# Kernel optimization log

Hardware: AMD Instinct MI355X
Metric: run time of the kernel (lower is better)

The kernel has to match this reference:

```python
import jax, jax.numpy as jnp
import numpy as np

N_NODES = 100000
N_EDGES = 1600000
IN_C, HID_C, OUT_C = 128, 256, 128


def setup_inputs() -> dict:
    key = jax.random.key(0)
    ks = jax.random.split(key, 6)
    x = jax.random.normal(ks[0], (N_NODES, IN_C), dtype=jnp.float32)
    edge_index = jax.random.randint(ks[1], (2, N_EDGES), 0, N_NODES, dtype=jnp.int64)
    s = 0.05
    W1a = jax.random.normal(ks[2], (IN_C, HID_C), dtype=jnp.float32) * s
    b1a = jnp.zeros((HID_C,), dtype=jnp.float32)
    W2a = jax.random.normal(ks[3], (HID_C, HID_C), dtype=jnp.float32) * s
    b2a = jnp.zeros((HID_C,), dtype=jnp.float32)
    W1b = jax.random.normal(ks[4], (HID_C, HID_C), dtype=jnp.float32) * s
    b1b = jnp.zeros((HID_C,), dtype=jnp.float32)
    W2b = jax.random.normal(ks[5], (HID_C, OUT_C), dtype=jnp.float32) * s
    b2b = jnp.zeros((OUT_C,), dtype=jnp.float32)
    return {"x": x, "edge_index": edge_index, "W1a": W1a, "b1a": b1a,
            "W2a": W2a, "b2a": b2a, "W1b": W1b, "b1b": b1b,
            "W2b": W2b, "b2b": b2b}


def _gin_conv(x, src, dst, W1, b1, W2, b2):
    # GINConv (eps=0): nn( x + sum_{j in N(i)} x_j )
    agg = jax.ops.segment_sum(x[src], dst, num_segments=N_NODES)  # [N, d]
    h = x + agg
    h = jnp.maximum(h @ W1 + b1, 0.0)
    return h @ W2 + b2


def reference(x, edge_index, W1a, b1a, W2a, b2a, W1b, b1b, W2b, b2b):
    src, dst = edge_index[0], edge_index[1]
    h = jnp.maximum(_gin_conv(x, src, dst, W1a, b1a, W2a, b2a), 0.0)  # relu(conv1)
    # dropout is identity in eval mode
    out = _gin_conv(h, src, dst, W1b, b1b, W2b, b2b)  # conv2
    return out
```

## Files before the change

kernel.cpp:

```cpp
#include <hip/hip_runtime.h>


#define N_NODES 100000
#define N_EDGES 1600000
#define NBUCK 13

typedef unsigned short ushort_t;
typedef short bf16x8 __attribute__((ext_vector_type(8)));
typedef float floatx4 __attribute__((ext_vector_type(4)));

static __device__ __forceinline__ ushort_t f2bf(float f) {
    unsigned u = __float_as_uint(f);
    u = (u + 0x7FFFu + ((u >> 16) & 1u)) >> 16;
    return (ushort_t)u;
}
static __device__ __forceinline__ unsigned pack2bf(float lo, float hi) {
    return (unsigned)f2bf(lo) | ((unsigned)f2bf(hi) << 16);
}
static __device__ __forceinline__ void addu4(float* acc, const uint4 v) {
    const unsigned w0 = v.x, w1 = v.y, w2 = v.z, w3 = v.w;
    acc[0] += __uint_as_float(w0 << 16);
    acc[1] += __uint_as_float(w0 & 0xFFFF0000u);
    acc[2] += __uint_as_float(w1 << 16);
    acc[3] += __uint_as_float(w1 & 0xFFFF0000u);
    acc[4] += __uint_as_float(w2 << 16);
    acc[5] += __uint_as_float(w2 & 0xFFFF0000u);
    acc[6] += __uint_as_float(w3 << 16);
    acc[7] += __uint_as_float(w3 & 0xFFFF0000u);
}

#define GLOAD_LDS16(g, l)                                                     \
    __builtin_amdgcn_global_load_lds(                                         \
        (const __attribute__((address_space(1))) void*)(g),                   \
        (__attribute__((address_space(3))) void*)(l), 16, 0, 0)

#define NX8 (N_NODES * 128 / 8)
__global__ __launch_bounds__(256) void cvt_fused_kernel(
    const float* __restrict__ X, ushort_t* __restrict__ Xb,
    const float* __restrict__ W1a, const float* __restrict__ W2a,
    const float* __restrict__ W1b, const float* __restrict__ W2b,
    ushort_t* __restrict__ wt1a, ushort_t* __restrict__ wt2a,
    ushort_t* __restrict__ wt1b, ushort_t* __restrict__ wt2b) {
    int i = blockIdx.x * 256 + threadIdx.x;
    if (i < NX8) {
        const float4 a = ((const float4*)X)[2 * i];
        const float4 b = ((const float4*)X)[2 * i + 1];
        uint4 r;
        r.x = pack2bf(a.x, a.y);
        r.y = pack2bf(a.z, a.w);
        r.z = pack2bf(b.x, b.y);
        r.w = pack2bf(b.z, b.w);
        ((uint4*)Xb)[i] = r;
        return;
    }
    i -= NX8;
    if (i < 32768) {
        int k = i >> 8, n = i & 255;
        wt1a[n * 128 + k] = f2bf(W1a[i]);
    } else if (i < 98304) {
        int j = i - 32768, k = j >> 8, n = j & 255;
        wt2a[n * 256 + k] = f2bf(W2a[j]);
    } else if (i < 163840) {
        int j = i - 98304, k = j >> 8, n = j & 255;
        wt1b[n * 256 + k] = f2bf(W1b[j]);
    } else if (i < 196608) {
        int j = i - 163840, k = j >> 7, n = j & 127;
        wt2b[n * 256 + k] = f2bf(W2b[j]);
    }
}

__global__ __launch_bounds__(256) void hist_kernel(const int* __restrict__ src,
                                                   const int* __restrict__ dst,
                                                   int* __restrict__ deg, int nE) {
    for (int e = blockIdx.x * 256 + threadIdx.x; e < nE; e += gridDim.x * 256) {
        int d = dst[e];
        int s = src[e];
        if ((unsigned)d < (unsigned)N_NODES && (unsigned)s < (unsigned)N_NODES)
            atomicAdd(&deg[d], 1);
    }
}

__global__ __launch_bounds__(256) void fill_kernel(const int* __restrict__ src,
                                                   const int* __restrict__ dst,
                                                   int* __restrict__ cursor,
                                                   int* __restrict__ csr_src, int nE) {
    const int bucket = blockIdx.y;
    for (int e = blockIdx.x * 256 + threadIdx.x; e < nE; e += gridDim.x * 256) {
        int d = dst[e];
        int s = src[e];
        if ((unsigned)d < (unsigned)N_NODES && (unsigned)s < (unsigned)N_NODES &&
            (d >> 13) == bucket) {
            int pos = atomicAdd(&cursor[d], 1);
            csr_src[pos] = s;
        }
    }
}

__global__ __launch_bounds__(256) void scan1_kernel(const int* __restrict__ deg,
                                                    int* __restrict__ bsum, int n) {
    __shared__ int l[256];
    int b = blockIdx.x, t = threadIdx.x;
    int base = b * 1024 + t * 4;
    int s = 0;
#pragma unroll
    for (int k = 0; k < 4; ++k) {
        int i = base + k;
        if (i < n) s += deg[i];
    }
    l[t] = s;
    __syncthreads();
    for (int off = 128; off > 0; off >>= 1) {
        if (t < off) l[t] += l[t + off];
        __syncthreads();
    }
    if (t == 0) bsum[b] = l[0];
}

__global__ __launch_bounds__(128) void scan2_kernel(const int* __restrict__ bsum,
                                                    int* __restrict__ boff, int nb) {
    __shared__ int l[128];
    int t = threadIdx.x;
    int v = (t < nb) ? bsum[t] : 0;
    l[t] = v;
    __syncthreads();
    for (int off = 1; off < 128; off <<= 1) {
        int add = (t >= off) ? l[t - off] : 0;
        __syncthreads();
        l[t] += add;
        __syncthreads();
    }
    if (t < nb) boff[t] = l[t] - v;
}

__global__ __launch_bounds__(256) void scan3_kernel(const int* __restrict__ deg,
                                                    const int* __restrict__ boff,
                                                    int* __restrict__ row_ptr,
                                                    int* __restrict__ cursor, int n) {
    __shared__ int l[256];
    int b = blockIdx.x, t = threadIdx.x;
    int base = b * 1024 + t * 4;
    int d[4];
    int s = 0;
#pragma unroll
    for (int k = 0; k < 4; ++k) {
        int i = base + k;
        d[k] = (i < n) ? deg[i] : 0;
        s += d[k];
    }
    l[t] = s;
    __syncthreads();
    for (int off = 1; off < 256; off <<= 1) {
        int add = (t >= off) ? l[t - off] : 0;
        __syncthreads();
        l[t] += add;
        __syncthreads();
    }
    int run = boff[b] + l[t] - s;
#pragma unroll
    for (int k = 0; k < 4; ++k) {
        int i = base + k;
        if (i < n) {
            row_ptr[i] = run;
            cursor[i] = run;
        }
        run += d[k];
    }
}

template <int C, int U>
__global__ __launch_bounds__(256) void agg_gather_kernel(
    const ushort_t* __restrict__ X, ushort_t* __restrict__ T,
    const int* __restrict__ row_ptr, const int* __restrict__ deg,
    const int* __restrict__ csr_src, const ushort_t* __restrict__ zrow, int nN) {
    constexpr int G = C / 8;
    constexpr int NPW = 64 / G;
    constexpr int B = U * NPW;
    const int lane = threadIdx.x & 63;
    const int wid = threadIdx.x >> 6;
    const int node = blockIdx.x * 4 + wid;
    if (node >= nN) return;
    const int sub = lane / G;
    const int coff = (lane % G) * 8;

    float acc[8];
#pragma unroll
    for (int k = 0; k < 8; ++k) acc[k] = 0.f;

    const int base = row_ptr[node];
    const int dg = deg[node];
    for (int j0 = 0; j0 < dg; j0 += 64) {
        int cnt = dg - j0;
        if (cnt > 64) cnt = 64;
        int nidx = (lane < cnt) ? csr_src[base + j0 + lane] : 0;
        if ((unsigned)nidx >= (unsigned)N_NODES) nidx = 0;
        for (int j = 0; j < cnt; j += B) {
            uint4 v[U];
#pragma unroll
            for (int u = 0; u < U; ++u) {
                int jj = j + u * NPW + sub;
                bool ok = jj < cnt;
                int idx = __shfl(nidx, ok ? jj : 0);
                const ushort_t* p = ok ? (X + (size_t)idx * C) : zrow;
                v[u] = *(const uint4*)(p + coff);
            }
#pragma unroll
            for (int u = 0; u < U; ++u) addu4(acc, v[u]);
        }
    }
    if (sub == 0) {
        uint4 v = *(const uint4*)(X + (size_t)node * C + coff);
        addu4(acc, v);
    }
#pragma unroll
    for (int off = G; off < 64; off <<= 1)
#pragma unroll
        for (int k = 0; k < 8; ++k) acc[k] += __shfl_xor(acc[k], off);

    if (lane < G) {
        uint4 r;
        r.x = pack2bf(acc[0], acc[1]);
        r.y = pack2bf(acc[2], acc[3]);
        r.z = pack2bf(acc[4], acc[5]);
        r.w = pack2bf(acc[6], acc[7]);
        *(uint4*)(T + (size_t)node * C + coff) = r;
    }
}

template <int K1, int N2, bool RELU2, typename OT>
__global__ __launch_bounds__(256, 3) void mlp_kernel(
    const ushort_t* __restrict__ A, const ushort_t* __restrict__ Wt1,
    const float* __restrict__ b1, const ushort_t* __restrict__ Wt2,
    const float* __restrict__ b2, OT* __restrict__ C, int M) {
    constexpr int N1 = 256, BM = 64, BK = 32;
    constexpr int NPW2 = N2 / 4;
    constexpr int RN2 = NPW2 / 16;
    __shared__ ushort_t As[BM * BK];
    __shared__ ushort_t Bs[N1 * BK];
    __shared__ ushort_t U[BM * N1];

    const int lane = threadIdx.x & 63;
    const int wid = threadIdx.x >> 6;
    const int l15 = lane & 15;
    const int q = lane >> 4;
    const int srow = lane >> 2;
    const int scol = (lane & 3) * 8;
    const int bm = blockIdx.x * BM;

    floatx4 acc[4][4];
#pragma unroll
    for (int mi = 0; mi < 4; ++mi)
#pragma unroll
        for (int ni = 0; ni < 4; ++ni) {
            floatx4 z = {0.f, 0.f, 0.f, 0.f};
            acc[mi][ni] = z;
        }

    for (int kt = 0; kt < K1; kt += BK) {
        {
            const int gr = bm + wid * 16 + srow;
            if (gr < M)
                GLOAD_LDS16(A + (size_t)gr * K1 + kt + scol, &As[(wid * 16) * BK]);
        }
#pragma unroll
        for (int u = 0; u < 4; ++u) {
            const int row = wid * 64 + u * 16;
            GLOAD_LDS16(Wt1 + (size_t)(row + srow) * K1 + kt + scol, &Bs[row * BK]);
        }
        __syncthreads();
        bf16x8 av[4], bv[4];
#pragma unroll
        for (int mi = 0; mi < 4; ++mi)
            av[mi] = *(const bf16x8*)&Bs[(wid * 64 + mi * 16 + l15) * BK + q * 8];
#pragma unroll
        for (int ni = 0; ni < 4; ++ni)
            bv[ni] = *(const bf16x8*)&As[(ni * 16 + l15) * BK + q * 8];
#pragma unroll
        for (int mi = 0; mi < 4; ++mi)
#pragma unroll
            for (int ni = 0; ni < 4; ++ni)
                acc[mi][ni] = __builtin_amdgcn_mfma_f32_16x16x32_bf16(
                    av[mi], bv[ni], acc[mi][ni], 0, 0, 0);
        __syncthreads();
    }

#pragma unroll
    for (int mi = 0; mi < 4; ++mi) {
        const int h0 = wid * 64 + mi * 16 + q * 4;
        const float4 b4 = *(const float4*)&b1[h0];
#pragma unroll
        for (int ni = 0; ni < 4; ++ni) {
            const int node = ni * 16 + l15;
            float v0 = acc[mi][ni][0] + b4.x; v0 = v0 > 0.f ? v0 : 0.f;
            float v1 = acc[mi][ni][1] + b4.y; v1 = v1 > 0.f ? v1 : 0.f;
            float v2 = acc[mi][ni][2] + b4.z; v2 = v2 > 0.f ? v2 : 0.f;
            float v3 = acc[mi][ni][3] + b4.w; v3 = v3 > 0.f ? v3 : 0.f;
            uint2 w;
            w.x = pack2bf(v0, v1);
            w.y = pack2bf(v2, v3);
            int byte = node * (N1 * 2) + h0 * 2;
            byte ^= (node & 7) << 4;
            *(uint2*)((char*)U + byte) = w;
        }
    }
    __syncthreads();

#pragma unroll
    for (int mi = 0; mi < 4; ++mi)
#pragma unroll
        for (int ni = 0; ni < 4; ++ni) {
            floatx4 z = {0.f, 0.f, 0.f, 0.f};
            acc[mi][ni] = z;
        }

    for (int kt = 0; kt < N1; kt += BK) {
#pragma unroll
        for (int u = 0; u < RN2; ++u) {
            const int row = wid * NPW2 + u * 16;
            GLOAD_LDS16(Wt2 + (size_t)(row + srow) * N1 + kt + scol, &Bs[row * BK]);
        }
        __syncthreads();
        bf16x8 av[4], bv[RN2];
#pragma unroll
        for (int mi = 0; mi < 4; ++mi) {
            const int node = mi * 16 + l15;
            const int byte =
                (node * (N1 * 2) + kt * 2 + q * 16) ^ ((node & 7) << 4);
            av[mi] = *(const bf16x8*)((const char*)U + byte);
        }
#pragma unroll
        for (int ni = 0; ni < RN2; ++ni)
            bv[ni] = *(const bf16x8*)&Bs[(wid * NPW2 + ni * 16 + l15) * BK + q * 8];
#pragma unroll
        for (int mi = 0; mi < 4; ++mi)
#pragma unroll
            for (int ni = 0; ni < RN2; ++ni)
                acc[mi][ni] = __builtin_amdgcn_mfma_f32_16x16x32_bf16(
                    av[mi], bv[ni], acc[mi][ni], 0, 0, 0);
        __syncthreads();
    }

    float bval[RN2];
#pragma unroll
    for (int ni = 0; ni < RN2; ++ni) bval[ni] = b2[wid * NPW2 + ni * 16 + l15];
#pragma unroll
    for (int mi = 0; mi < 4; ++mi) {
#pragma unroll
        for (int r = 0; r < 4; ++r) {
            const int row = bm + mi * 16 + q * 4 + r;
            if (row < M) {
#pragma unroll
                for (int ni = 0; ni < RN2; ++ni) {
                    const int col = wid * NPW2 + ni * 16 + l15;
                    float v = acc[mi][ni][r] + bval[ni];
                    if (RELU2) v = v > 0.f ? v : 0.f;
                    if constexpr (sizeof(OT) == 2)
                        C[(size_t)row * N2 + col] = f2bf(v);
                    else
                        C[(size_t)row * N2 + col] = v;
                }
            }
        }
    }
}

extern "C" void kernel_launch(void* const* d_in, const int* in_sizes, int n_in,
                              void* d_out, int out_size, void* d_ws, size_t ws_size,
                              hipStream_t stream) {
    const float* x   = (const float*)d_in[0];
    const int*   ei  = (const int*)d_in[1];
    const float* W1a = (const float*)d_in[2];
    const float* b1a = (const float*)d_in[3];
    const float* W2a = (const float*)d_in[4];
    const float* b2a = (const float*)d_in[5];
    const float* W1b = (const float*)d_in[6];
    const float* b1b = (const float*)d_in[7];
    const float* W2b = (const float*)d_in[8];
    const float* b2b = (const float*)d_in[9];
    const int* src = ei;
    const int* dst = ei + N_EDGES;
    float* out = (float*)d_out;

    char* base = (char*)d_ws;
    size_t o = 0;
    ushort_t* wt1a = (ushort_t*)(base + o); o += 128 * 256 * 2;
    ushort_t* wt2a = (ushort_t*)(base + o); o += 256 * 256 * 2;
    ushort_t* wt1b = (ushort_t*)(base + o); o += 256 * 256 * 2;
    ushort_t* wt2b = (ushort_t*)(base + o); o += 256 * 128 * 2;
    o = (o + 255) & ~(size_t)255;
    ushort_t* zrow = (ushort_t*)(base + o); o += 512;
    int* deg     = (int*)(base + o); o += (size_t)N_NODES * 4;
    int* row_ptr = (int*)(base + o); o += (size_t)N_NODES * 4;
    int* cursor  = (int*)(base + o); o += (size_t)N_NODES * 4;
    int* bsum    = (int*)(base + o); o += 128 * 4;
    int* boff    = (int*)(base + o); o += 128 * 4;
    o = (o + 255) & ~(size_t)255;
    int* csr_src = (int*)(base + o); o += (size_t)N_EDGES * 4;
    o = (o + 255) & ~(size_t)255;
    ushort_t* t1   = (ushort_t*)(base + o); o += (size_t)N_NODES * 128 * 2;
    ushort_t* tbig = (ushort_t*)(base + o); o += (size_t)N_NODES * 256 * 2;
    o += 128 * 1024;
    (void)ws_size; (void)o; (void)in_sizes; (void)n_in; (void)out_size;

    ushort_t* inter = (ushort_t*)d_out;
    ushort_t* xb    = (ushort_t*)d_out;

    cvt_fused_kernel<<<(NX8 + 196608 + 255) / 256, 256, 0, stream>>>(
        x, xb, W1a, W2a, W1b, W2b, wt1a, wt2a, wt1b, wt2b);

    const int NB = (N_NODES + 1023) / 1024;
    hipMemsetAsync(zrow, 0, 512 + (size_t)N_NODES * 4, stream);
    hist_kernel<<<2048, 256, 0, stream>>>(src, dst, deg, N_EDGES);
    scan1_kernel<<<NB, 256, 0, stream>>>(deg, bsum, N_NODES);
    scan2_kernel<<<1, 128, 0, stream>>>(bsum, boff, NB);
    scan3_kernel<<<NB, 256, 0, stream>>>(deg, boff, row_ptr, cursor, N_NODES);
    fill_kernel<<<dim3(1024, NBUCK), 256, 0, stream>>>(src, dst, cursor, csr_src,
                                                       N_EDGES);

    const int ga = (N_NODES + 3) / 4;
    const int gf = (N_NODES + 63) / 64;

    agg_gather_kernel<128, 4><<<ga, 256, 0, stream>>>(xb, t1, row_ptr, deg,
                                                      csr_src, zrow, N_NODES);
    mlp_kernel<128, 256, true, ushort_t><<<gf, 256, 0, stream>>>(
        t1, wt1a, b1a, wt2a, b2a, inter, N_NODES);

    agg_gather_kernel<256, 8><<<ga, 256, 0, stream>>>(inter, tbig, row_ptr,
                                                      deg, csr_src, zrow, N_NODES);
    mlp_kernel<256, 128, false, float><<<gf, 256, 0, stream>>>(
        tbig, wt1b, b1b, wt2b, b2b, out, N_NODES);
}
```

Measured before the change: 532.4 us.

## Fuse histogram into convert kernel, merge scan passes, pack row_ptr/deg, raise gather unroll

Folds the degree histogram into the fused convert kernel and merges scan2 into scan3, with each block reducing the preceding block sums itself. This removes two kernel launches. It also stores row_ptr and degree as a packed int2 so the gather kernels do one load per node, and doubles the gather unroll factor (U) for both layers to keep more loads in flight. The trade-off is that every scan3 block redundantly re-reduces the block sums, and the higher unroll raises register pressure.

```diff
diff --git a/kernel.cpp b/kernel.cpp
--- a/kernel.cpp
+++ b/kernel.cpp
@@ -35,12 +35,16 @@
         (__attribute__((address_space(3))) void*)(l), 16, 0, 0)
 
 #define NX8 (N_NODES * 128 / 8)
+#define CVT_TOTAL (NX8 + 196608)
+#define HIST_THREADS (2048 * 256)
 __global__ __launch_bounds__(256) void cvt_fused_kernel(
     const float* __restrict__ X, ushort_t* __restrict__ Xb,
     const float* __restrict__ W1a, const float* __restrict__ W2a,
     const float* __restrict__ W1b, const float* __restrict__ W2b,
     ushort_t* __restrict__ wt1a, ushort_t* __restrict__ wt2a,
-    ushort_t* __restrict__ wt1b, ushort_t* __restrict__ wt2b) {
+    ushort_t* __restrict__ wt1b, ushort_t* __restrict__ wt2b,
+    const int* __restrict__ src, const int* __restrict__ dst,
+    int* __restrict__ deg, int nE) {
     int i = blockIdx.x * 256 + threadIdx.x;
     if (i < NX8) {
         const float4 a = ((const float4*)X)[2 * i];
@@ -53,26 +57,24 @@
         ((uint4*)Xb)[i] = r;
         return;
     }
-    i -= NX8;
-    if (i < 32768) {
-        int k = i >> 8, n = i & 255;
-        wt1a[n * 128 + k] = f2bf(W1a[i]);
-    } else if (i < 98304) {
-        int j = i - 32768, k = j >> 8, n = j & 255;
-        wt2a[n * 256 + k] = f2bf(W2a[j]);
-    } else if (i < 163840) {
-        int j = i - 98304, k = j >> 8, n = j & 255;
-        wt1b[n * 256 + k] = f2bf(W1b[j]);
-    } else if (i < 196608) {
-        int j = i - 163840, k = j >> 7, n = j & 127;
-        wt2b[n * 256 + k] = f2bf(W2b[j]);
-    }
-}
-
-__global__ __launch_bounds__(256) void hist_kernel(const int* __restrict__ src,
-                                                   const int* __restrict__ dst,
-                                                   int* __restrict__ deg, int nE) {
-    for (int e = blockIdx.x * 256 + threadIdx.x; e < nE; e += gridDim.x * 256) {
+    if (i < CVT_TOTAL) {
+        i -= NX8;
+        if (i < 32768) {
+            int k = i >> 8, n = i & 255;
+            wt1a[n * 128 + k] = f2bf(W1a[i]);
+        } else if (i < 98304) {
+            int j = i - 32768, k = j >> 8, n = j & 255;
+            wt2a[n * 256 + k] = f2bf(W2a[j]);
+        } else if (i < 163840) {
+            int j = i - 98304, k = j >> 8, n = j & 255;
+            wt1b[n * 256 + k] = f2bf(W1b[j]);
+        } else {
+            int j = i - 163840, k = j >> 7, n = j & 127;
+            wt2b[n * 256 + k] = f2bf(W2b[j]);
+        }
+        return;
+    }
+    for (int e = i - CVT_TOTAL; e < nE; e += HIST_THREADS) {
         int d = dst[e];
         int s = src[e];
         if ((unsigned)d < (unsigned)N_NODES && (unsigned)s < (unsigned)N_NODES)
@@ -116,28 +118,23 @@
     if (t == 0) bsum[b] = l[0];
 }
 
-__global__ __launch_bounds__(128) void scan2_kernel(const int* __restrict__ bsum,
-                                                    int* __restrict__ boff, int nb) {
-    __shared__ int l[128];
-    int t = threadIdx.x;
-    int v = (t < nb) ? bsum[t] : 0;
-    l[t] = v;
+__global__ __launch_bounds__(256) void scan3_kernel(const int* __restrict__ deg,
+                                                    const int* __restrict__ bsum,
+                                                    int* __restrict__ row_ptr,
+                                                    int* __restrict__ cursor,
+                                                    int2* __restrict__ rpd,
+                                                    int n, int nb) {
+    __shared__ int l[256];
+    __shared__ int boffs;
+    int b = blockIdx.x, t = threadIdx.x;
+    l[t] = (t < b && t < nb) ? bsum[t] : 0;
     __syncthreads();
-    for (int off = 1; off < 128; off <<= 1) {
-        int add = (t >= off) ? l[t - off] : 0;
-        __syncthreads();
-        l[t] += add;
-        __syncthreads();
-    }
-    if (t < nb) boff[t] = l[t] - v;
-}
-
-__global__ __launch_bounds__(256) void scan3_kernel(const int* __restrict__ deg,
-                                                    const int* __restrict__ boff,
-                                                    int* __restrict__ row_ptr,
-                                                    int* __restrict__ cursor, int n) {
-    __shared__ int l[256];
-    int b = blockIdx.x, t = threadIdx.x;
+    for (int off = 128; off > 0; off >>= 1) {
+        if (t < off) l[t] += l[t + off];
+        __syncthreads();
+    }
+    if (t == 0) boffs = l[0];
+    __syncthreads();
     int base = b * 1024 + t * 4;
     int d[4];
     int s = 0;
@@ -155,13 +152,14 @@
         l[t] += add;
         __syncthreads();
     }
-    int run = boff[b] + l[t] - s;
+    int run = boffs + l[t] - s;
 #pragma unroll
     for (int k = 0; k < 4; ++k) {
         int i = base + k;
         if (i < n) {
             row_ptr[i] = run;
             cursor[i] = run;
+            rpd[i] = make_int2(run, d[k]);
         }
         run += d[k];
     }
@@ -170,8 +168,8 @@
 template <int C, int U>
 __global__ __launch_bounds__(256) void agg_gather_kernel(
     const ushort_t* __restrict__ X, ushort_t* __restrict__ T,
-    const int* __restrict__ row_ptr, const int* __restrict__ deg,
-    const int* __restrict__ csr_src, const ushort_t* __restrict__ zrow, int nN) {
+    const int2* __restrict__ rpd, const int* __restrict__ csr_src,
+    const ushort_t* __restrict__ zrow, int nN) {
     constexpr int G = C / 8;
     constexpr int NPW = 64 / G;
     constexpr int B = U * NPW;
@@ -186,8 +184,9 @@
 #pragma unroll
     for (int k = 0; k < 8; ++k) acc[k] = 0.f;
 
-    const int base = row_ptr[node];
-    const int dg = deg[node];
+    const int2 rd = rpd[node];
+    const int base = rd.x;
+    const int dg = rd.y;
     for (int j0 = 0; j0 < dg; j0 += 64) {
         int cnt = dg - j0;
         if (cnt > 64) cnt = 64;
@@ -392,7 +391,8 @@
     int* row_ptr = (int*)(base + o); o += (size_t)N_NODES * 4;
     int* cursor  = (int*)(base + o); o += (size_t)N_NODES * 4;
     int* bsum    = (int*)(base + o); o += 128 * 4;
-    int* boff    = (int*)(base + o); o += 128 * 4;
+    o = (o + 255) & ~(size_t)255;
+    int2* rpd    = (int2*)(base + o); o += (size_t)N_NODES * 8;
     o = (o + 255) & ~(size_t)255;
     int* csr_src = (int*)(base + o); o += (size_t)N_EDGES * 4;
     o = (o + 255) & ~(size_t)255;
@@ -404,28 +404,28 @@
     ushort_t* inter = (ushort_t*)d_out;
     ushort_t* xb    = (ushort_t*)d_out;
 
-    cvt_fused_kernel<<<(NX8 + 196608 + 255) / 256, 256, 0, stream>>>(
-        x, xb, W1a, W2a, W1b, W2b, wt1a, wt2a, wt1b, wt2b);
+    hipMemsetAsync(zrow, 0, 512 + (size_t)N_NODES * 4, stream);
+
+    cvt_fused_kernel<<<CVT_TOTAL / 256 + 2048, 256, 0, stream>>>(
+        x, xb, W1a, W2a, W1b, W2b, wt1a, wt2a, wt1b, wt2b, src, dst, deg, N_EDGES);
 
     const int NB = (N_NODES + 1023) / 1024;
-    hipMemsetAsync(zrow, 0, 512 + (size_t)N_NODES * 4, stream);
-    hist_kernel<<<2048, 256, 0, stream>>>(src, dst, deg, N_EDGES);
     scan1_kernel<<<NB, 256, 0, stream>>>(deg, bsum, N_NODES);
-    scan2_kernel<<<1, 128, 0, stream>>>(bsum, boff, NB);
-    scan3_kernel<<<NB, 256, 0, stream>>>(deg, boff, row_ptr, cursor, N_NODES);
+    scan3_kernel<<<NB, 256, 0, stream>>>(deg, bsum, row_ptr, cursor, rpd,
+                                         N_NODES, NB);
     fill_kernel<<<dim3(1024, NBUCK), 256, 0, stream>>>(src, dst, cursor, csr_src,
                                                        N_EDGES);
 
     const int ga = (N_NODES + 3) / 4;
     const int gf = (N_NODES + 63) / 64;
 
-    agg_gather_kernel<128, 4><<<ga, 256, 0, stream>>>(xb, t1, row_ptr, deg,
-                                                      csr_src, zrow, N_NODES);
+    agg_gather_kernel<128, 8><<<ga, 256, 0, stream>>>(xb, t1, rpd, csr_src,
+                                                      zrow, N_NODES);
     mlp_kernel<128, 256, true, ushort_t><<<gf, 256, 0, stream>>>(
         t1, wt1a, b1a, wt2a, b2a, inter, N_NODES);
 
-    agg_gather_kernel<256, 8><<<ga, 256, 0, stream>>>(inter, tbig, row_ptr,
-                                                      deg, csr_src, zrow, N_NODES);
+    agg_gather_kernel<256, 16><<<ga, 256, 0, stream>>>(inter, tbig, rpd,
+                                                       csr_src, zrow, N_NODES);
     mlp_kernel<256, 128, false, float><<<gf, 256, 0, stream>>>(
         tbig, wt1b, b1b, wt2b, b2b, out, N_NODES);
 }
```

New measurement: 538.2 us. No clear change (+1.1%).
